# Optimization experiments

Hardware: AMD Instinct MI355X
Metric: run time of the kernel (lower is better)

## Reference

```python
import jax, jax.numpy as jnp
import numpy as np

B, D, H, O, E = 16384, 1024, 512, 256, 8


def setup_inputs() -> dict:
    key = jax.random.key(0)
    ks = jax.random.split(key, 8)
    s = lambda k, shape, fan: (jax.random.normal(k, shape, jnp.float32) / np.sqrt(fan).astype(np.float32))
    z = lambda shape: jnp.zeros(shape, jnp.float32)
    return {
        "x": jax.random.normal(ks[0], (B, D), jnp.float32),
        # gating network: D -> 256 -> 128 -> E
        "gw1": s(ks[1], (D, 256), D), "gb1": z((256,)),
        "gw2": s(ks[2], (256, 128), 256), "gb2": z((128,)),
        "gw3": s(ks[3], (128, E), 128), "gb3": z((E,)),
        # experts, batched over expert dim E: D -> H -> H -> O
        "ew1": s(ks[4], (E, D, H), D), "eb1": z((E, H)),
        "ew2": s(ks[5], (E, H, H), H), "eb2": z((E, H)),
        "ew3": s(ks[6], (E, H, O), H), "eb3": z((E, O)),
    }


def reference(x, gw1, gb1, gw2, gb2, gw3, gb3, ew1, eb1, ew2, eb2, ew3, eb3):
    # Gating network (dropout is identity in eval mode)
    g = jax.nn.relu(x @ gw1 + gb1)
    g = jax.nn.relu(g @ gw2 + gb2)
    gates = jax.nn.softmax(g @ gw3 + gb3, axis=1)  # [B, E]
    # All experts run on every token: batched small MLPs over expert axis e
    h = jax.nn.relu(jnp.einsum('bd,edh->ebh', x, ew1) + eb1[:, None, :])   # [E, B, H]
    h = jax.nn.relu(jnp.einsum('ebh,ehk->ebk', h, ew2) + eb2[:, None, :])  # [E, B, H]
    eo = jnp.einsum('ebh,eho->ebo', h, ew3) + eb3[:, None, :]              # [E, B, O]
    # gate-weighted sum over experts
    out = jnp.einsum('ebo,be->bo', eo, gates)  # [B, O]
    return out
```

## Files before the change

### kernel.cpp

```cpp
#include <hip/hip_runtime.h>
#include <hip/hip_bf16.h>

typedef __hip_bfloat16 bf16;
typedef __attribute__((ext_vector_type(8))) __bf16 bf16x8;
typedef __attribute__((ext_vector_type(4))) float f32x4;

#define B_ 16384
#define D_ 1024
#define H_ 512
#define O_ 256
#define E_ 8
#define BC_ 8192
#define NG_ (E_ * H_ + 256)

static_assert(B_ % BC_ == 0, "chunking");

#define GLDS(src, dst) __builtin_amdgcn_global_load_lds( \
    (const __attribute__((address_space(1))) void*)(src), \
    (__attribute__((address_space(3))) void*)(dst), 16, 0, 0)

#define BAR()   asm volatile("s_barrier" ::: "memory")
#define LGKM0() do { asm volatile("s_waitcnt lgkmcnt(0)" ::: "memory"); \
                     __builtin_amdgcn_sched_barrier(0); } while (0)

__global__ void detect_k(const unsigned short* __restrict__ x, int* __restrict__ flag) {
    __shared__ int s;
    if (threadIdx.x == 0) s = 0;
    __syncthreads();
    int big = 0;
    for (int i = threadIdx.x; i < 2048; i += 256)
        if (((x[i] >> 7) & 0xFF) >= 150) big = 1;
    if (big) atomicOr(&s, 1);
    __syncthreads();
    if (threadIdx.x == 0) *flag = s;
}

__global__ void preproc_k(const void* x, bf16* xc,
                          const void* gb1, const void* gb2, const void* gw3,
                          const void* gb3, const void* eb1, const void* eb2,
                          const void* eb3,
                          bf16* gb1c, bf16* gb2c, bf16* gw3c, bf16* gb3c,
                          bf16* eb1c, bf16* eb2c, bf16* eb3c,
                          const void* gw1, const void* gw2,
                          const void* ew1, const void* ew2, const void* ew3,
                          bf16* gw1t, bf16* gw2t,
                          bf16* ew1t, bf16* ew2t, bf16* ew3t,
                          long ew3_zout, long ew3_cstride,
                          const int* __restrict__ flag) {
    const int f = *flag;
    const int tid = threadIdx.y * 32 + threadIdx.x;
    int lin = blockIdx.x;

    if (lin < 1024) {
        const long n8 = (long)B_ * D_ / 8;
        long i = (long)lin * 256 + tid;
        const long stride = 1024 * 256;
        if (f) {
            const float4* s = (const float4*)x;
            for (; i < n8; i += stride) {
                float4 a = s[2 * i], b = s[2 * i + 1];
                bf16 tmp[8];
                tmp[0] = __float2bfloat16(a.x); tmp[1] = __float2bfloat16(a.y);
                tmp[2] = __float2bfloat16(a.z); tmp[3] = __float2bfloat16(a.w);
                tmp[4] = __float2bfloat16(b.x); tmp[5] = __float2bfloat16(b.y);
                tmp[6] = __float2bfloat16(b.z); tmp[7] = __float2bfloat16(b.w);
                *(uint4*)(xc + i * 8) = *(const uint4*)tmp;
            }
        } else {
            const uint4* s = (const uint4*)x;
            for (; i < n8; i += stride) *(uint4*)(xc + i * 8) = s[i];
        }
        return;
    }
    if (lin < 1031) {
        const int id = lin - 1024;
        const void* sp[7] = {gb1, gb2, gw3, gb3, eb1, eb2, eb3};
        bf16* dp[7] = {gb1c, gb2c, gw3c, gb3c, eb1c, eb2c, eb3c};
        const int len[7] = {256, 128, 1024, 8, E_ * H_, E_ * H_, E_ * O_};
        const float* sf = (const float*)sp[id];
        const bf16*  sb = (const bf16*)sp[id];
        bf16* d = dp[id];
        for (int i = tid; i < len[id]; i += 256)
            d[i] = f ? __float2bfloat16(sf[i]) : sb[i];
        return;
    }
    lin -= 1031;
    __shared__ bf16 t[32][33];
    const void* src; bf16* dst; int R, C, bx, by, bz; long z_out, c_stride;
    if (lin < 256) {
        src = gw1; dst = gw1t; R = 1024; C = 256; z_out = 0; c_stride = 1024;
        bx = lin & 7; by = lin >> 3; bz = 0;
    } else if (lin < 288) {
        lin -= 256;
        src = gw2; dst = gw2t; R = 256; C = 128; z_out = 0; c_stride = 256;
        bx = lin & 3; by = lin >> 2; bz = 0;
    } else if (lin < 4384) {
        lin -= 288;
        src = ew1; dst = ew1t; R = 1024; C = 512;
        z_out = (long)H_ * D_; c_stride = D_;
        bx = lin & 15; by = (lin >> 4) & 31; bz = lin >> 9;
    } else if (lin < 6432) {
        lin -= 4384;
        src = ew2; dst = ew2t; R = 512; C = 512;
        z_out = (long)H_ * H_; c_stride = H_;
        bx = lin & 15; by = (lin >> 4) & 15; bz = lin >> 8;
    } else {
        lin -= 6432;
        src = ew3; dst = ew3t; R = 512; C = 256;
        z_out = ew3_zout; c_stride = ew3_cstride;
        bx = lin & 7; by = (lin >> 3) & 15; bz = lin >> 7;
    }
    const long zi = (long)bz * R * C;
    const int xg = bx * 32 + threadIdx.x;
    const int y0 = by * 32;
    const float* inf = (const float*)src;
    const bf16* inb = (const bf16*)src;
#pragma unroll
    for (int i = 0; i < 4; i++) {
        int r = y0 + threadIdx.y + i * 8;
        long idx = zi + (long)r * C + xg;
        t[threadIdx.y + i * 8][threadIdx.x] =
            f ? __float2bfloat16(inf[idx]) : inb[idx];
    }
    __syncthreads();
    const int xr = by * 32 + threadIdx.x;
    const long zo = (long)bz * z_out;
#pragma unroll
    for (int i = 0; i < 4; i++) {
        int c = bx * 32 + threadIdx.y + i * 8;
        dst[zo + (long)c * c_stride + xr] = t[threadIdx.x][threadIdx.y + i * 8];
    }
}

__global__ void gate3_softmax_k(const bf16* __restrict__ g2,
                                const bf16* __restrict__ gw3,
                                const bf16* __restrict__ gb3,
                                float* __restrict__ gates) {
    __shared__ float w[128 * 8];
    __shared__ float bsh[8];
    const int tid = threadIdx.x;
    for (int i = tid; i < 1024; i += 256) w[i] = __bfloat162float(gw3[i]);
    if (tid < 8) bsh[tid] = __bfloat162float(gb3[tid]);
    __syncthreads();

    const long row = (long)blockIdx.x * 256 + tid;
    float acc[8];
#pragma unroll
    for (int o = 0; o < 8; o++) acc[o] = bsh[o];

    const bf16x8* rp8 = (const bf16x8*)(g2 + row * 128);
#pragma unroll 4
    for (int c8 = 0; c8 < 16; c8++) {
        bf16x8 v8 = rp8[c8];
#pragma unroll
        for (int jj = 0; jj < 8; jj++) {
            float v = (float)v8[jj];
            int k = c8 * 8 + jj;
#pragma unroll
            for (int o = 0; o < 8; o++) acc[o] += v * w[k * 8 + o];
        }
    }
    float m = acc[0];
#pragma unroll
    for (int o = 1; o < 8; o++) m = fmaxf(m, acc[o]);
    float s = 0.f;
#pragma unroll
    for (int o = 0; o < 8; o++) { acc[o] = __expf(acc[o] - m); s += acc[o]; }
    const float inv = 1.f / s;
#pragma unroll
    for (int o = 0; o < 8; o++) gates[row * 8 + o] = acc[o] * inv;
}

template <int MODE>
__global__ __launch_bounds__(256, 4)
void gemm_bt(const bf16* __restrict__ A, const bf16* __restrict__ Bt,
             const bf16* __restrict__ bias, const float* __restrict__ gates,
             void* __restrict__ Cout, const bf16* __restrict__ eb3,
             int lda, int ldb, int ldo, int K,
             long a_z, long b_z, long bias_z, long out_z,
             int e_gate, int k_per_e, long a_e, long b_e, long row0) {
    __shared__ __attribute__((aligned(16))) bf16 As[128 * 32];
    __shared__ __attribute__((aligned(16))) bf16 Bs[128 * 32];

    const int tid  = threadIdx.x;
    const int lane = tid & 63;
    const int quad = lane >> 4;
    const int l15  = lane & 15;
    const int wid  = tid >> 6;
    const int wr   = (wid >> 1) << 6;
    const int wc   = (wid & 1) << 6;
    const int z    = blockIdx.z;
    const long m0  = (long)blockIdx.y << 7;
    const long n0  = (long)blockIdx.x << 7;

    const bf16* Az = A + (long)z * a_z;
    const bf16* Bz = Bt + (long)z * b_z;

    f32x4 acc[4][4];
#pragma unroll
    for (int i = 0; i < 4; i++)
#pragma unroll
        for (int j = 0; j < 4; j++) acc[i][j] = (f32x4){0.f, 0.f, 0.f, 0.f};

    const int erow = tid >> 2;
    const int ecol = (tid & 3) << 3;

    const int n_e   = k_per_e ? (K / k_per_e) : 1;
    const int inner = (k_per_e ? k_per_e : K) >> 5;

    for (int e = 0; e < n_e; e++) {
        const bf16* Ae = Az + (long)e * a_e;
        const bf16* Be = Bz + (long)e * b_e;
        for (int kti = 0; kti < inner; kti++) {
            const int kk = kti << 5;
#pragma unroll
            for (int i = 0; i < 2; i++) {
                const int r = (i << 6) + erow;
                GLDS(Ae + (m0 + r) * lda + (kk + ecol), As + r * 32 + ecol);
            }
#pragma unroll
            for (int i = 0; i < 2; i++) {
                const int r = (i << 6) + erow;
                GLDS(Be + (n0 + r) * ldb + (kk + ecol), Bs + r * 32 + ecol);
            }
            __syncthreads();
            bf16x8 af[4], bfr[4];
#pragma unroll
            for (int i = 0; i < 4; i++)
                af[i] = *(const bf16x8*)(As + (wr + i * 16 + l15) * 32 + (quad << 3));
#pragma unroll
            for (int j = 0; j < 4; j++)
                bfr[j] = *(const bf16x8*)(Bs + (wc + j * 16 + l15) * 32 + (quad << 3));
#pragma unroll
            for (int i = 0; i < 4; i++)
#pragma unroll
                for (int j = 0; j < 4; j++)
                    acc[i][j] = __builtin_amdgcn_mfma_f32_16x16x32_bf16(
                        af[i], bfr[j], acc[i][j], 0, 0, 0);
            __syncthreads();
        }
    }

    const int eg = (e_gate >= 0) ? e_gate : z;

    if constexpr (MODE == 0 || MODE == 1) {
        bf16* C = (bf16*)Cout + (long)z * out_z;
        const bf16* bb = bias + (long)z * bias_z;
        float gv[4][4];
        if constexpr (MODE == 1) {
#pragma unroll
            for (int i = 0; i < 4; i++)
#pragma unroll
                for (int rg = 0; rg < 4; rg++)
                    gv[i][rg] = gates[(row0 + m0 + wr + i * 16 + quad * 4 + rg) * 8 + eg];
        }
#pragma unroll
        for (int j = 0; j < 4; j++) {
            const int c = (int)n0 + wc + j * 16 + l15;
            const float bv = __bfloat162float(bb[c]);
#pragma unroll
            for (int i = 0; i < 4; i++) {
#pragma unroll
                for (int rg = 0; rg < 4; rg++) {
                    const long r = m0 + wr + i * 16 + quad * 4 + rg;
                    float v = fmaxf(acc[i][j][rg] + bv, 0.f);
                    if constexpr (MODE == 1) v *= gv[i][rg];
                    C[r * ldo + c] = __float2bfloat16(v);
                }
            }
        }
    } else if constexpr (MODE == 2) {
        float* C = (float*)Cout;
#pragma unroll
        for (int i = 0; i < 4; i++) {
#pragma unroll
            for (int rg = 0; rg < 4; rg++) {
                const long r = m0 + wr + i * 16 + quad * 4 + rg;
                const float g = gates[(row0 + r) * 8 + eg];
#pragma unroll
                for (int j = 0; j < 4; j++) {
                    const int c = (int)n0 + wc + j * 16 + l15;
                    const float b3 = __bfloat162float(eb3[eg * O_ + c]);
                    C[r * ldo + c] += acc[i][j][rg] + g * b3;
                }
            }
        }
    }
}

template <int MODE>
__global__ __launch_bounds__(512, 2)
void gemm256(const bf16* __restrict__ A, const bf16* __restrict__ Bt,
             const bf16* __restrict__ bias, const float* __restrict__ gates,
             void* __restrict__ Cout, const bf16* __restrict__ eb3,
             int lda, int ldb, int ldo, int K,
             long a_z, long b_z, long bias_z, long out_z, long row0) {
    __shared__ __attribute__((aligned(16))) bf16 lds[2][2][256 * 64];

    int bx = blockIdx.x, by = blockIdx.y;
    {
        const int gx = gridDim.x;
        const int nwg = gx * gridDim.y;
        if ((nwg & 7) == 0) {
            int lin = bx + gx * by;
            lin = (lin & 7) * (nwg >> 3) + (lin >> 3);
            bx = lin % gx; by = lin / gx;
        }
    }

    const int tid  = threadIdx.x;
    const int lane = tid & 63;
    const int quad = lane >> 4;
    const int l15  = lane & 15;
    const int w    = tid >> 6;
    const int wm   = w >> 2;
    const int wn   = w & 3;
    const int z    = blockIdx.z;
    const long m0  = (long)by << 8;
    const long n0  = (long)bx << 8;

    const bf16* __restrict__ Az = A + z * a_z;
    const bf16* __restrict__ Bz = Bt + z * b_z;

    f32x4 acc[8][4];
#pragma unroll
    for (int i = 0; i < 8; ++i)
#pragma unroll
        for (int j = 0; j < 4; ++j) acc[i][j] = (f32x4){0.f, 0.f, 0.f, 0.f};

    bf16x8 af[4][2], bv[2][2];

    auto stage = [&](int buf, int mat, int half, int kt) {
        const bf16* __restrict__ G = mat ? Bz : Az;
        const int ld = mat ? ldb : lda;
        const long p0 = mat ? n0 : m0;
#pragma unroll
        for (int l = 0; l < 2; ++l) {
            const int ci = (w << 1) | l;
            const int rb = mat ? ((ci >> 2) << 6) + (half << 5) + ((ci & 3) << 3)
                               : ((ci >> 3) << 7) + (half << 6) + ((ci & 7) << 3);
            const int row = rb + (lane >> 3);
            const int cb  = ((lane & 7) << 4) ^ ((row & 7) << 4);
            GLDS(G + (p0 + row) * ld + kt * 64 + (cb >> 1),
                 &lds[buf][mat][rb * 64]);
        }
    };
    auto ldaf = [&](int buf, int qm) {
#pragma unroll
        for (int i = 0; i < 4; ++i) {
            const int r = (wm << 7) + (qm << 6) + (i << 4) + l15;
            const char* p = (const char*)&lds[buf][0][r * 64];
            const int sw = (r & 7) << 4;
#pragma unroll
            for (int s = 0; s < 2; ++s)
                af[i][s] = *(const bf16x8*)(p + (((s << 6) + (quad << 4)) ^ sw));
        }
    };
    auto ldbf = [&](int buf, int qn) {
#pragma unroll
        for (int j = 0; j < 2; ++j) {
            const int r = (wn << 6) + (qn << 5) + (j << 4) + l15;
            const char* p = (const char*)&lds[buf][1][r * 64];
            const int sw = (r & 7) << 4;
#pragma unroll
            for (int s = 0; s < 2; ++s)
                bv[j][s] = *(const bf16x8*)(p + (((s << 6) + (quad << 4)) ^ sw));
        }
    };
    auto mmac = [&](int qm, int qn) {
#pragma unroll
        for (int i = 0; i < 4; ++i)
#pragma unroll
            for (int j = 0; j < 2; ++j)
#pragma unroll
                for (int s = 0; s < 2; ++s)
                    acc[(qm << 2) + i][(qn << 1) + j] =
                        __builtin_amdgcn_mfma_f32_16x16x32_bf16(
                            af[i][s], bv[j][s], acc[(qm << 2) + i][(qn << 1) + j],
                            0, 0, 0);
    };

    const int nt = K >> 6;

    stage(0, 0, 0, 0); stage(0, 0, 1, 0); stage(0, 1, 0, 0); stage(0, 1, 1, 0);
    stage(1, 0, 0, 1); stage(1, 1, 0, 1);
    asm volatile("s_waitcnt vmcnt(4)" ::: "memory");
    BAR();

    const int hi = nt >> 1;
    for (int it = 0; it < hi; ++it) {
        const int t1k = 2 * it + 1, t2k = 2 * it + 2, t3k = 2 * it + 3;
        const bool do2 = t2k < nt, do3 = t3k < nt;
        ldaf(0, 0); ldbf(0, 0); stage(1, 0, 1, t1k);
        BAR(); LGKM0();
        __builtin_amdgcn_s_setprio(1); mmac(0, 0); __builtin_amdgcn_s_setprio(0);
        BAR();
        ldbf(0, 1); stage(1, 1, 1, t1k);
        BAR(); LGKM0();
        __builtin_amdgcn_s_setprio(1); mmac(0, 1); __builtin_amdgcn_s_setprio(0);
        BAR();
        ldaf(0, 1); ldbf(0, 0); if (do2) stage(0, 0, 0, t2k);
        BAR(); LGKM0();
        __builtin_amdgcn_s_setprio(1); mmac(1, 0); __builtin_amdgcn_s_setprio(0);
        BAR();
        ldbf(0, 1); if (do2) stage(0, 1, 0, t2k);
        BAR(); LGKM0();
        __builtin_amdgcn_s_setprio(1); mmac(1, 1); __builtin_amdgcn_s_setprio(0);
        if (do2) { asm volatile("s_waitcnt vmcnt(4)" ::: "memory"); }
        else     { asm volatile("s_waitcnt vmcnt(0)" ::: "memory"); }
        BAR();
        ldaf(1, 0); ldbf(1, 0); if (do2) stage(0, 0, 1, t2k);
        BAR(); LGKM0();
        __builtin_amdgcn_s_setprio(1); mmac(0, 0); __builtin_amdgcn_s_setprio(0);
        BAR();
        ldbf(1, 1); if (do2) stage(0, 1, 1, t2k);
        BAR(); LGKM0();
        __builtin_amdgcn_s_setprio(1); mmac(0, 1); __builtin_amdgcn_s_setprio(0);
        BAR();
        ldaf(1, 1); ldbf(1, 0); if (do3) stage(1, 0, 0, t3k);
        BAR(); LGKM0();
        __builtin_amdgcn_s_setprio(1); mmac(1, 0); __builtin_amdgcn_s_setprio(0);
        BAR();
        ldbf(1, 1); if (do3) stage(1, 1, 0, t3k);
        BAR(); LGKM0();
        __builtin_amdgcn_s_setprio(1); mmac(1, 1); __builtin_amdgcn_s_setprio(0);
        if (do3) { asm volatile("s_waitcnt vmcnt(4)" ::: "memory"); }
        else     { asm volatile("s_waitcnt vmcnt(0)" ::: "memory"); }
        BAR();
    }

    if constexpr (MODE == 0 || MODE == 1) {
        bf16* C = (bf16*)Cout + z * out_z;
        const bf16* bb = bias + z * bias_z;
        float bvv[4];
#pragma unroll
        for (int jg = 0; jg < 4; ++jg)
            bvv[jg] = __bfloat162float(bb[(int)n0 + (wn << 6) + (jg << 4) + l15]);
#pragma unroll
        for (int ig = 0; ig < 8; ++ig) {
#pragma unroll
            for (int rg = 0; rg < 4; ++rg) {
                const long r = m0 + (wm << 7) + (ig << 4) + (quad << 2) + rg;
                float g = 1.f;
                if constexpr (MODE == 1) g = gates[(row0 + r) * 8 + z];
#pragma unroll
                for (int jg = 0; jg < 4; ++jg) {
                    const int c = (int)n0 + (wn << 6) + (jg << 4) + l15;
                    float v = fmaxf(acc[ig][jg][rg] + bvv[jg], 0.f);
                    if constexpr (MODE == 1) v *= g;
                    C[r * ldo + c] = __float2bfloat16(v);
                }
            }
        }
    } else if constexpr (MODE == 4) {
        float* C = (float*)Cout + z * out_z;
        float b3v[4];
#pragma unroll
        for (int jg = 0; jg < 4; ++jg)
            b3v[jg] = __bfloat162float(eb3[z * O_ + (int)n0 + (wn << 6) + (jg << 4) + l15]);
#pragma unroll
        for (int ig = 0; ig < 8; ++ig) {
#pragma unroll
            for (int rg = 0; rg < 4; ++rg) {
                const long r = m0 + (wm << 7) + (ig << 4) + (quad << 2) + rg;
                const float g = gates[(row0 + r) * 8 + z];
#pragma unroll
                for (int jg = 0; jg < 4; ++jg) {
                    const int c = (int)n0 + (wn << 6) + (jg << 4) + l15;
                    C[r * ldo + c] = acc[ig][jg][rg] + g * b3v[jg];
                }
            }
        }
    } else {
        float* C = (float*)Cout + z * out_z;
        const int e0 = z << 1;
        float b30[4], b31[4];
#pragma unroll
        for (int jg = 0; jg < 4; ++jg) {
            const int c = (int)n0 + (wn << 6) + (jg << 4) + l15;
            b30[jg] = __bfloat162float(eb3[e0 * O_ + c]);
            b31[jg] = __bfloat162float(eb3[(e0 + 1) * O_ + c]);
        }
#pragma unroll
        for (int ig = 0; ig < 8; ++ig) {
#pragma unroll
            for (int rg = 0; rg < 4; ++rg) {
                const long r = m0 + (wm << 7) + (ig << 4) + (quad << 2) + rg;
                const float g0 = gates[(row0 + r) * 8 + e0];
                const float g1 = gates[(row0 + r) * 8 + e0 + 1];
#pragma unroll
                for (int jg = 0; jg < 4; ++jg) {
                    const int c = (int)n0 + (wn << 6) + (jg << 4) + l15;
                    C[r * ldo + c] = acc[ig][jg][rg] + g0 * b30[jg] + g1 * b31[jg];
                }
            }
        }
    }
}

__global__ void zero_f32_k(float* __restrict__ p) {
    p[(long)blockIdx.x * 256 + threadIdx.x] = 0.f;
}
__global__ void out_cvt_k(const float* __restrict__ in, void* __restrict__ out,
                          const int* __restrict__ flag) {
    const long i = (long)blockIdx.x * 256 + threadIdx.x;
    if (*flag) ((float*)out)[i] = in[i];
    else       ((bf16*)out)[i] = __float2bfloat16(in[i]);
}
template <int NZ>
__global__ void reduceN_k(const float* __restrict__ p, void* __restrict__ out,
                          const int* __restrict__ flag, long n, long off) {
    const long i = ((long)blockIdx.x * 256 + threadIdx.x) * 4;
    float4 s = *(const float4*)(p + i);
#pragma unroll
    for (int zz = 1; zz < NZ; ++zz) {
        float4 a = *(const float4*)(p + (long)zz * n + i);
        s.x += a.x; s.y += a.y; s.z += a.z; s.w += a.w;
    }
    if (*flag) {
        *(float4*)((float*)out + off + i) = s;
    } else {
        bf16* o = (bf16*)out + off + i;
        o[0] = __float2bfloat16(s.x); o[1] = __float2bfloat16(s.y);
        o[2] = __float2bfloat16(s.z); o[3] = __float2bfloat16(s.w);
    }
}

extern "C" void kernel_launch(void* const* d_in, const int* in_sizes, int n_in,
                              void* d_out, int out_size, void* d_ws, size_t ws_size,
                              hipStream_t stream) {
    (void)in_sizes; (void)n_in; (void)out_size;
    const void* x   = d_in[0];
    const void* gw1 = d_in[1];
    const void* gb1 = d_in[2];
    const void* gw2 = d_in[3];
    const void* gb2 = d_in[4];
    const void* gw3 = d_in[5];
    const void* gb3 = d_in[6];
    const void* ew1 = d_in[7];
    const void* eb1 = d_in[8];
    const void* ew2 = d_in[9];
    const void* eb2 = d_in[10];
    const void* ew3 = d_in[11];
    const void* eb3 = d_in[12];

    char* ws = (char*)d_ws;
    size_t off = 0;
    auto alloc = [&](size_t n) { char* p = ws + off; off += (n + 255) & ~(size_t)255; return p; };

    int*  flag  = (int*)alloc(256);
    bf16* xc    = (bf16*)alloc((size_t)B_ * D_ * 2);
    bf16* ew1g  = (bf16*)alloc((size_t)NG_ * D_ * 2);
    bf16* ew1t  = ew1g;
    bf16* gw1t  = ew1g + (size_t)E_ * H_ * D_;
    bf16* gw2t  = (bf16*)alloc((size_t)128 * 256 * 2);
    bf16* ew2t  = (bf16*)alloc((size_t)E_ * H_ * H_ * 2);
    bf16* ew3t  = (bf16*)alloc((size_t)E_ * O_ * H_ * 2);
    bf16* eb1g  = (bf16*)alloc((size_t)NG_ * 2);
    bf16* eb1c  = eb1g;
    bf16* gb1c  = eb1g + E_ * H_;
    bf16* gb2c  = (bf16*)alloc(128 * 2);
    bf16* gw3c  = (bf16*)alloc(1024 * 2);
    bf16* gb3c  = (bf16*)alloc(8 * 2);
    bf16* eb2c  = (bf16*)alloc((size_t)E_ * H_ * 2);
    bf16* eb3c  = (bf16*)alloc((size_t)E_ * O_ * 2);
    bf16* g2b   = (bf16*)alloc((size_t)B_ * 128 * 2);
    float* gates = (float*)alloc((size_t)B_ * 8 * 4);

    const size_t smallCore = off;
    const size_t needBig = smallCore + ((size_t)B_ * NG_ * 2 + 256)
                                     + ((size_t)B_ * E_ * H_ * 2 + 256) + 4096;
    const size_t g1sz = (size_t)B_ * 256 * 2 + 256;
    const size_t needPair = smallCore + g1sz + ((size_t)E_ * BC_ * H_ * 2 + 256)
                                      + ((size_t)B_ * E_ * H_ * 2 + 256)
                                      + (4ull * B_ * O_ * 4 + 256) + 4096;
    const size_t needChunk = smallCore + g1sz + ((size_t)E_ * BC_ * H_ * 2 + 256)
                                       + ((size_t)BC_ * E_ * H_ * 2 + 256)
                                       + (8ull * BC_ * O_ * 4 + 256) + 4096;
    const bool pathBig   = ws_size >= needBig;
    const bool pathPair  = ws_size >= needPair;
    const bool pathChunk = ws_size >= needChunk;

    detect_k<<<1, 256, 0, stream>>>((const unsigned short*)x, flag);

    const long e3zo = pathChunk ? (long)H_ : (long)O_ * H_;
    const long e3cs = pathChunk ? (long)E_ * H_ : (long)H_;
    preproc_k<<<8487, dim3(32, 8), 0, stream>>>(
        x, xc, gb1, gb2, gw3, gb3, eb1, eb2, eb3,
        gb1c, gb2c, gw3c, gb3c, eb1c, eb2c, eb3c,
        gw1, gw2, ew1, ew2, ew3, gw1t, gw2t, ew1t, ew2t, ew3t,
        e3zo, e3cs, flag);

    if (pathBig) {
        bf16* h1g = (bf16*)alloc((size_t)B_ * NG_ * 2);
        bf16* h2  = (bf16*)alloc((size_t)B_ * E_ * H_ * 2);
        float* parts = (float*)h1g;

        gemm256<0><<<dim3(NG_ / 256, B_ / 256, 1), 512, 0, stream>>>(
            xc, ew1g, eb1g, nullptr, h1g, nullptr,
            D_, D_, NG_, D_,
            0, 0, 0, 0, 0);
        gemm_bt<0><<<dim3(1, 128, 1), 256, 0, stream>>>(
            h1g + (size_t)E_ * H_, gw2t, gb2c, nullptr, g2b, nullptr,
            NG_, 256, 128, 256, 0, 0, 0, 0, 0, 0, 0, 0, 0);
        gate3_softmax_k<<<dim3(B_ / 256), 256, 0, stream>>>(g2b, gw3c, gb3c, gates);
        gemm256<1><<<dim3(2, B_ / 256, 8), 512, 0, stream>>>(
            h1g, ew2t, eb2c, gates, h2, nullptr,
            NG_, H_, E_ * H_, H_,
            (long)H_, (long)H_ * H_, (long)H_, (long)H_, 0);
        gemm256<5><<<dim3(1, B_ / 256, 4), 512, 0, stream>>>(
            h2, ew3t, nullptr, gates, parts, eb3c,
            E_ * H_, E_ * H_, O_, 1024,
            2L * H_, 2L * H_, 0, (long)B_ * O_, 0);
        reduceN_k<4><<<dim3(B_ * O_ / 1024), 256, 0, stream>>>(
            parts, d_out, flag, (long)B_ * O_, 0L);
        return;
    }

    bf16* g1 = (bf16*)alloc((size_t)B_ * 256 * 2);
    gemm_bt<0><<<dim3(2, 128, 1), 256, 0, stream>>>(
        xc, gw1t, gb1c, nullptr, g1, nullptr,
        1024, 1024, 256, 1024, 0, 0, 0, 0, 0, 0, 0, 0, 0);
    gemm_bt<0><<<dim3(1, 128, 1), 256, 0, stream>>>(
        g1, gw2t, gb2c, nullptr, g2b, nullptr,
        256, 256, 128, 256, 0, 0, 0, 0, 0, 0, 0, 0, 0);
    gate3_softmax_k<<<dim3(B_ / 256), 256, 0, stream>>>(g2b, gw3c, gb3c, gates);

    if (pathChunk) {
        bf16* h1c = (bf16*)alloc((size_t)E_ * BC_ * H_ * 2);
        bf16* h2  = pathPair
                  ? (bf16*)alloc((size_t)B_ * E_ * H_ * 2)
                  : (bf16*)alloc((size_t)BC_ * E_ * H_ * 2);
        float* parts = pathPair
                     ? (float*)alloc(4ull * B_ * O_ * 4)
                     : (float*)alloc(8ull * BC_ * O_ * 4);

        for (int ch = 0; ch < B_ / BC_; ch++) {
            const long rb = (long)ch * BC_;
            gemm256<0><<<dim3(2, BC_ / 256, 8), 512, 0, stream>>>(
                xc + rb * D_, ew1t, eb1c, nullptr, h1c, nullptr,
                D_, D_, H_, D_,
                0, (long)H_ * D_, (long)H_, (long)BC_ * H_, 0);
            bf16* h2dst = pathPair ? (h2 + rb * (long)E_ * H_) : h2;
            gemm256<1><<<dim3(2, BC_ / 256, 8), 512, 0, stream>>>(
                h1c, ew2t, eb2c, gates, h2dst, nullptr,
                H_, H_, E_ * H_, H_,
                (long)BC_ * H_, (long)H_ * H_, (long)H_, (long)H_, rb);
            if (!pathPair) {
                gemm256<4><<<dim3(1, BC_ / 256, 8), 512, 0, stream>>>(
                    h2, ew3t, nullptr, gates, parts, eb3c,
                    E_ * H_, E_ * H_, O_, 512,
                    (long)H_, (long)H_, 0, (long)BC_ * O_, rb);
                reduceN_k<8><<<dim3(BC_ * O_ / 1024), 256, 0, stream>>>(
                    parts, d_out, flag, (long)BC_ * O_, rb * O_);
            }
        }
        if (pathPair) {
            gemm256<5><<<dim3(1, B_ / 256, 4), 512, 0, stream>>>(
                h2, ew3t, nullptr, gates, parts, eb3c,
                E_ * H_, E_ * H_, O_, 1024,
                2L * H_, 2L * H_, 0, (long)B_ * O_, 0);
            reduceN_k<4><<<dim3(B_ * O_ / 1024), 256, 0, stream>>>(
                parts, d_out, flag, (long)B_ * O_, 0L);
        }
    } else {
        bf16* h1s = (bf16*)alloc((size_t)B_ * H_ * 2);
        bf16* h2s = (bf16*)alloc((size_t)B_ * H_ * 2);
        float* oacc = (float*)alloc((size_t)B_ * O_ * 4);
        zero_f32_k<<<dim3(B_ * O_ / 256), 256, 0, stream>>>(oacc);
        for (int e = 0; e < E_; e++) {
            gemm_bt<0><<<dim3(4, 128, 1), 256, 0, stream>>>(
                xc, ew1t + (size_t)e * H_ * D_, eb1c + (size_t)e * H_, nullptr, h1s, nullptr,
                1024, 1024, 512, 1024, 0, 0, 0, 0, 0, 0, 0, 0, 0);
            gemm_bt<1><<<dim3(4, 128, 1), 256, 0, stream>>>(
                h1s, ew2t + (size_t)e * H_ * H_, eb2c + (size_t)e * H_, gates, h2s, nullptr,
                512, 512, 512, 512, 0, 0, 0, 0, e, 0, 0, 0, 0);
            gemm_bt<2><<<dim3(2, 128, 1), 256, 0, stream>>>(
                h2s, ew3t + (size_t)e * O_ * H_, nullptr, gates, oacc, eb3c,
                512, 512, 256, 512, 0, 0, 0, 0, e, 0, 0, 0, 0);
        }
        out_cvt_k<<<dim3(B_ * O_ / 256), 256, 0, stream>>>(oacc, d_out, flag);
    }
}
```

Measured before the change: 520.9 us.

## Chunk fused gate+expert first-layer GEMM over batch to fit smaller workspace

Replaces the full-batch fused path, which needed a [B, NG] hidden buffer, with a two-chunk loop. Each chunk runs the combined gate+expert layer-1 GEMM, the gate layers, softmax and the expert layer-2 GEMM, writing into a full-size h2. The layer-3 GEMM plus reduction then runs once over the whole batch, with its partial sums aliased into the chunk buffer. This lets the fused single-pass layer 1 run when the workspace is too small for the old full-batch path. It also drops the separate pair variant, so the chunk path always does per-chunk layer 3 and reduction. The cost is extra kernel launches and smaller per-launch grids.

After: 542.3 us. 4.1% more time.

```diff
diff --git a/kernel.cpp b/kernel.cpp
--- a/kernel.cpp
+++ b/kernel.cpp
@@ -568,46 +568,48 @@
     float* gates = (float*)alloc((size_t)B_ * 8 * 4);
 
     const size_t smallCore = off;
-    const size_t needBig = smallCore + ((size_t)B_ * NG_ * 2 + 256)
-                                     + ((size_t)B_ * E_ * H_ * 2 + 256) + 4096;
+    const size_t needFused = smallCore + ((size_t)BC_ * NG_ * 2 + 256)
+                                       + ((size_t)B_ * E_ * H_ * 2 + 256) + 4096;
     const size_t g1sz = (size_t)B_ * 256 * 2 + 256;
-    const size_t needPair = smallCore + g1sz + ((size_t)E_ * BC_ * H_ * 2 + 256)
-                                      + ((size_t)B_ * E_ * H_ * 2 + 256)
-                                      + (4ull * B_ * O_ * 4 + 256) + 4096;
     const size_t needChunk = smallCore + g1sz + ((size_t)E_ * BC_ * H_ * 2 + 256)
                                        + ((size_t)BC_ * E_ * H_ * 2 + 256)
                                        + (8ull * BC_ * O_ * 4 + 256) + 4096;
-    const bool pathBig   = ws_size >= needBig;
-    const bool pathPair  = ws_size >= needPair;
+    const bool pathFused = ws_size >= needFused;
     const bool pathChunk = ws_size >= needChunk;
 
     detect_k<<<1, 256, 0, stream>>>((const unsigned short*)x, flag);
 
-    const long e3zo = pathChunk ? (long)H_ : (long)O_ * H_;
-    const long e3cs = pathChunk ? (long)E_ * H_ : (long)H_;
+    const bool l3pair = pathFused || pathChunk;
+    const long e3zo = l3pair ? (long)H_ : (long)O_ * H_;
+    const long e3cs = l3pair ? (long)E_ * H_ : (long)H_;
     preproc_k<<<8487, dim3(32, 8), 0, stream>>>(
         x, xc, gb1, gb2, gw3, gb3, eb1, eb2, eb3,
         gb1c, gb2c, gw3c, gb3c, eb1c, eb2c, eb3c,
         gw1, gw2, ew1, ew2, ew3, gw1t, gw2t, ew1t, ew2t, ew3t,
         e3zo, e3cs, flag);
 
-    if (pathBig) {
-        bf16* h1g = (bf16*)alloc((size_t)B_ * NG_ * 2);
-        bf16* h2  = (bf16*)alloc((size_t)B_ * E_ * H_ * 2);
-        float* parts = (float*)h1g;
-
-        gemm256<0><<<dim3(NG_ / 256, B_ / 256, 1), 512, 0, stream>>>(
-            xc, ew1g, eb1g, nullptr, h1g, nullptr,
-            D_, D_, NG_, D_,
-            0, 0, 0, 0, 0);
-        gemm_bt<0><<<dim3(1, 128, 1), 256, 0, stream>>>(
-            h1g + (size_t)E_ * H_, gw2t, gb2c, nullptr, g2b, nullptr,
-            NG_, 256, 128, 256, 0, 0, 0, 0, 0, 0, 0, 0, 0);
-        gate3_softmax_k<<<dim3(B_ / 256), 256, 0, stream>>>(g2b, gw3c, gb3c, gates);
-        gemm256<1><<<dim3(2, B_ / 256, 8), 512, 0, stream>>>(
-            h1g, ew2t, eb2c, gates, h2, nullptr,
-            NG_, H_, E_ * H_, H_,
-            (long)H_, (long)H_ * H_, (long)H_, (long)H_, 0);
+    if (pathFused) {
+        bf16* h1gc = (bf16*)alloc((size_t)BC_ * NG_ * 2);
+        bf16* h2   = (bf16*)alloc((size_t)B_ * E_ * H_ * 2);
+        float* parts = (float*)h1gc;
+
+        for (int ch = 0; ch < B_ / BC_; ch++) {
+            const long rb = (long)ch * BC_;
+            gemm256<0><<<dim3(NG_ / 256, BC_ / 256, 1), 512, 0, stream>>>(
+                xc + rb * D_, ew1g, eb1g, nullptr, h1gc, nullptr,
+                D_, D_, NG_, D_,
+                0, 0, 0, 0, 0);
+            gemm_bt<0><<<dim3(1, BC_ / 128, 1), 256, 0, stream>>>(
+                h1gc + (size_t)E_ * H_, gw2t, gb2c, nullptr,
+                g2b + rb * 128, nullptr,
+                NG_, 256, 128, 256, 0, 0, 0, 0, 0, 0, 0, 0, 0);
+            gate3_softmax_k<<<dim3(BC_ / 256), 256, 0, stream>>>(
+                g2b + rb * 128, gw3c, gb3c, gates + rb * 8);
+            gemm256<1><<<dim3(2, BC_ / 256, 8), 512, 0, stream>>>(
+                h1gc, ew2t, eb2c, gates, h2 + rb * (long)E_ * H_, nullptr,
+                NG_, H_, E_ * H_, H_,
+                (long)H_, (long)H_ * H_, (long)H_, (long)H_, rb);
+        }
         gemm256<5><<<dim3(1, B_ / 256, 4), 512, 0, stream>>>(
             h2, ew3t, nullptr, gates, parts, eb3c,
             E_ * H_, E_ * H_, O_, 1024,
@@ -628,12 +630,8 @@
 
     if (pathChunk) {
         bf16* h1c = (bf16*)alloc((size_t)E_ * BC_ * H_ * 2);
-        bf16* h2  = pathPair
-                  ? (bf16*)alloc((size_t)B_ * E_ * H_ * 2)
-                  : (bf16*)alloc((size_t)BC_ * E_ * H_ * 2);
-        float* parts = pathPair
-                     ? (float*)alloc(4ull * B_ * O_ * 4)
-                     : (float*)alloc(8ull * BC_ * O_ * 4);
+        bf16* h2c = (bf16*)alloc((size_t)BC_ * E_ * H_ * 2);
+        float* parts = (float*)alloc(8ull * BC_ * O_ * 4);
 
         for (int ch = 0; ch < B_ / BC_; ch++) {
             const long rb = (long)ch * BC_;
@@ -641,27 +639,16 @@
                 xc + rb * D_, ew1t, eb1c, nullptr, h1c, nullptr,
                 D_, D_, H_, D_,
                 0, (long)H_ * D_, (long)H_, (long)BC_ * H_, 0);
-            bf16* h2dst = pathPair ? (h2 + rb * (long)E_ * H_) : h2;
             gemm256<1><<<dim3(2, BC_ / 256, 8), 512, 0, stream>>>(
-                h1c, ew2t, eb2c, gates, h2dst, nullptr,
+                h1c, ew2t, eb2c, gates, h2c, nullptr,
                 H_, H_, E_ * H_, H_,
                 (long)BC_ * H_, (long)H_ * H_, (long)H_, (long)H_, rb);
-            if (!pathPair) {
-                gemm256<4><<<dim3(1, BC_ / 256, 8), 512, 0, stream>>>(
-                    h2, ew3t, nullptr, gates, parts, eb3c,
-                    E_ * H_, E_ * H_, O_, 512,
-                    (long)H_, (long)H_, 0, (long)BC_ * O_, rb);
-                reduceN_k<8><<<dim3(BC_ * O_ / 1024), 256, 0, stream>>>(
-                    parts, d_out, flag, (long)BC_ * O_, rb * O_);
-            }
-        }
-        if (pathPair) {
-            gemm256<5><<<dim3(1, B_ / 256, 4), 512, 0, stream>>>(
-                h2, ew3t, nullptr, gates, parts, eb3c,
-                E_ * H_, E_ * H_, O_, 1024,
-                2L * H_, 2L * H_, 0, (long)B_ * O_, 0);
-            reduceN_k<4><<<dim3(B_ * O_ / 1024), 256, 0, stream>>>(
-                parts, d_out, flag, (long)B_ * O_, 0L);
+            gemm256<4><<<dim3(1, BC_ / 256, 8), 512, 0, stream>>>(
+                h2c, ew3t, nullptr, gates, parts, eb3c,
+                E_ * H_, E_ * H_, O_, 512,
+                (long)H_, (long)H_, 0, (long)BC_ * O_, rb);
+            reduceN_k<8><<<dim3(BC_ * O_ / 1024), 256, 0, stream>>>(
+                parts, d_out, flag, (long)BC_ * O_, rb * O_);
         }
     } else {
         bf16* h1s = (bf16*)alloc((size_t)B_ * H_ * 2);
```
